# Performance work log

Hardware: AMD Instinct MI355X
Metric: run time of the kernel (lower is better)

## Reference

```python
import jax, jax.numpy as jnp
import numpy as np

EPS = 1e-5


def setup_inputs() -> dict:
    key = jax.random.key(0)
    ks = jax.random.split(key, 6)
    B, IN, OUT = 32768, 128, 2048
    return {
        "x": jax.random.normal(ks[0], (B, IN), dtype=jnp.float32),
        "y": jax.random.normal(ks[1], (B, OUT), dtype=jnp.float32),
        "linear_w": jax.random.normal(ks[2], (OUT, IN), dtype=jnp.float32) * (1.0 / np.sqrt(IN)),
        "linear_b": jax.random.normal(ks[3], (OUT,), dtype=jnp.float32) * 0.02,
        "norm_w": jax.random.uniform(ks[4], (OUT,), dtype=jnp.float32),
        "norm_b": jax.random.normal(ks[5], (OUT,), dtype=jnp.float32) * 0.02,
    }


def reference(x, y, linear_w, linear_b, norm_w, norm_b):
    # Linear: [B, IN] @ [IN, OUT] + b -> [B, OUT]
    h = jnp.einsum("bi,oi->bo", x, linear_w) + linear_b
    # Instance norm per row over the feature dim (biased variance, matching kernel)
    mean = jnp.mean(h, axis=-1, keepdims=True)
    var = jnp.mean(h * h, axis=-1, keepdims=True) - mean * mean
    inv_std = jax.lax.rsqrt(var + EPS)
    normed = (h - mean) * inv_std * norm_w + norm_b
    # Fused add then mul with second tensor
    return (normed + y) * y
```

## Files before the change

### kernel.cpp

```cpp
#include <hip/hip_runtime.h>
#include <hip/hip_bf16.h>
#include <cstdint>
#include <cstddef>


#define IN_DIM  128
#define OUT_DIM 2048
#define ROWS    16
#define EPS     1e-5f

typedef short  short8  __attribute__((ext_vector_type(8)));
typedef float  floatx4 __attribute__((ext_vector_type(4)));

__device__ __forceinline__ unsigned short f2bf(float f) {
    union { float f; unsigned int u; } v; v.f = f;
    unsigned int u = v.u;
    u += 0x7fffu + ((u >> 16) & 1u);
    return (unsigned short)(u >> 16);
}

__global__ void convert_w_kernel(const float* __restrict__ w,
                                 unsigned short* __restrict__ wbf, int n) {
    int i = (blockIdx.x * blockDim.x + threadIdx.x) * 4;
    if (i < n) {
        float4 v = *(const float4*)(w + i);
        ushort4 o;
        o.x = f2bf(v.x); o.y = f2bf(v.y); o.z = f2bf(v.z); o.w = f2bf(v.w);
        *(ushort4*)(wbf + i) = o;
    }
}

__global__ __launch_bounds__(512)
void fused_linear_norm_kernel(const float* __restrict__ x,
                              const float* __restrict__ y,
                              const unsigned short* __restrict__ wbf,
                              const float* __restrict__ lb,
                              const float* __restrict__ nw,
                              const float* __restrict__ nb,
                              float* __restrict__ out) {
    const int tid  = threadIdx.x;
    const int wave = tid >> 6;
    const int lane = tid & 63;
    const int l15  = lane & 15;
    const int quad = lane >> 4;
    const int row0 = blockIdx.x * ROWS;

    short8 afrag[4];
    {
        const float* xr = x + (size_t)(row0 + l15) * IN_DIM + quad * 8;
        #pragma unroll
        for (int s = 0; s < 4; ++s) {
            float4 p0 = *(const float4*)(xr + s * 32);
            float4 p1 = *(const float4*)(xr + s * 32 + 4);
            short8 a;
            a[0] = (short)f2bf(p0.x); a[1] = (short)f2bf(p0.y);
            a[2] = (short)f2bf(p0.z); a[3] = (short)f2bf(p0.w);
            a[4] = (short)f2bf(p1.x); a[5] = (short)f2bf(p1.y);
            a[6] = (short)f2bf(p1.z); a[7] = (short)f2bf(p1.w);
            afrag[s] = a;
        }
    }

    floatx4 acc[16];
    const int c0 = wave * 256;
    #pragma unroll
    for (int t = 0; t < 16; ++t) {
        acc[t] = (floatx4){0.f, 0.f, 0.f, 0.f};
        const unsigned short* wp = wbf + (size_t)(c0 + t * 16 + l15) * IN_DIM + quad * 8;
        #pragma unroll
        for (int s = 0; s < 4; ++s) {
            short8 b = *(const short8*)(wp + s * 32);
            acc[t] = __builtin_amdgcn_mfma_f32_16x16x32_bf16(afrag[s], b, acc[t], 0, 0, 0);
        }
    }

    float s1[4] = {0.f, 0.f, 0.f, 0.f};
    float s2[4] = {0.f, 0.f, 0.f, 0.f};
    #pragma unroll
    for (int t = 0; t < 16; ++t) {
        int col = c0 + t * 16 + l15;
        float bv = lb[col];
        #pragma unroll
        for (int r = 0; r < 4; ++r) {
            float h = acc[t][r] + bv;
            acc[t][r] = h;
            s1[r] += h;
            s2[r] += h * h;
        }
    }

    #pragma unroll
    for (int off = 1; off < 16; off <<= 1) {
        #pragma unroll
        for (int r = 0; r < 4; ++r) {
            s1[r] += __shfl_xor(s1[r], off);
            s2[r] += __shfl_xor(s2[r], off);
        }
    }

    __shared__ float red1[8][ROWS];
    __shared__ float red2[8][ROWS];
    __shared__ float smean[ROWS], sinv[ROWS];
    if (l15 == 0) {
        #pragma unroll
        for (int r = 0; r < 4; ++r) {
            red1[wave][quad * 4 + r] = s1[r];
            red2[wave][quad * 4 + r] = s2[r];
        }
    }
    __syncthreads();
    if (tid < ROWS) {
        float t1 = 0.f, t2 = 0.f;
        #pragma unroll
        for (int w = 0; w < 8; ++w) { t1 += red1[w][tid]; t2 += red2[w][tid]; }
        float mean = t1 * (1.0f / OUT_DIM);
        float var  = t2 * (1.0f / OUT_DIM) - mean * mean;
        smean[tid] = mean;
        sinv[tid]  = rsqrtf(var + EPS);
    }
    __syncthreads();

    float mean[4], inv[4];
    #pragma unroll
    for (int r = 0; r < 4; ++r) {
        mean[r] = smean[quad * 4 + r];
        inv[r]  = sinv[quad * 4 + r];
    }

    __shared__ float stage[8][ROWS][68];
    #pragma unroll
    for (int c = 0; c < 4; ++c) {
        #pragma unroll
        for (int tl = 0; tl < 4; ++tl) {
            const int t   = c * 4 + tl;
            const int col = c0 + t * 16 + l15;
            const float gw = nw[col];
            const float gb = nb[col];
            #pragma unroll
            for (int r = 0; r < 4; ++r) {
                const float normed = (acc[t][r] - mean[r]) * inv[r] * gw + gb;
                stage[wave][quad * 4 + r][tl * 16 + l15] = normed;
            }
        }
        __asm__ volatile("s_waitcnt lgkmcnt(0)" ::: "memory");
        #pragma unroll
        for (int i = 0; i < 4; ++i) {
            const int rl = i * 4 + quad;
            const float4 v = *(const float4*)&stage[wave][rl][l15 * 4];
            const size_t idx = (size_t)(row0 + rl) * OUT_DIM + (c0 + c * 64 + l15 * 4);
            const float4 yv = *(const float4*)(y + idx);
            float4 o;
            o.x = (v.x + yv.x) * yv.x;
            o.y = (v.y + yv.y) * yv.y;
            o.z = (v.z + yv.z) * yv.z;
            o.w = (v.w + yv.w) * yv.w;
            *(float4*)(out + idx) = o;
        }
    }
}

extern "C" void kernel_launch(void* const* d_in, const int* in_sizes, int n_in,
                              void* d_out, int out_size, void* d_ws, size_t ws_size,
                              hipStream_t stream) {
    const float* x  = (const float*)d_in[0];
    const float* y  = (const float*)d_in[1];
    const float* lw = (const float*)d_in[2];
    const float* lb = (const float*)d_in[3];
    const float* nw = (const float*)d_in[4];
    const float* nb = (const float*)d_in[5];
    float* out = (float*)d_out;
    unsigned short* wbf = (unsigned short*)d_ws;

    const int wn = OUT_DIM * IN_DIM;
    convert_w_kernel<<<wn / 4 / 256, 256, 0, stream>>>(lw, wbf, wn);

    const int nblocks = 32768 / ROWS;
    fused_linear_norm_kernel<<<nblocks, 512, 0, stream>>>(x, y, wbf, lb, nw, nb, out);
}
```

Before: 544.7 us.

## Prefetch y into LDS via async global_load_lds overlapping the MFMA loop

Issues asynchronous global-to-LDS loads of the block's y tile, interleaved with the GEMM MFMA loop, so the y fetch overlaps compute. The epilogue then reads y from LDS and writes the output directly as scalar stores, dropping the float4 LDS staging. The large y buffer in LDS (~131KB) limits the CU to one block, and the scalar stores are less coalesced than the old float4 writes.

```diff
diff --git a/kernel.cpp b/kernel.cpp
--- a/kernel.cpp
+++ b/kernel.cpp
@@ -1,5 +1,4 @@
 #include <hip/hip_runtime.h>
-#include <hip/hip_bf16.h>
 #include <cstdint>
 #include <cstddef>
 
@@ -7,6 +6,7 @@
 #define IN_DIM  128
 #define OUT_DIM 2048
 #define ROWS    16
+#define YPITCH  2052
 #define EPS     1e-5f
 
 typedef short  short8  __attribute__((ext_vector_type(8)));
@@ -45,6 +45,11 @@
     const int quad = lane >> 4;
     const int row0 = blockIdx.x * ROWS;
 
+    __shared__ float ylds[ROWS * YPITCH];
+    __shared__ float red1[8][ROWS];
+    __shared__ float red2[8][ROWS];
+    __shared__ float smean[ROWS], sinv[ROWS];
+
     short8 afrag[4];
     {
         const float* xr = x + (size_t)(row0 + l15) * IN_DIM + quad * 8;
@@ -63,6 +68,7 @@
 
     floatx4 acc[16];
     const int c0 = wave * 256;
+    const float* ybase = y + (size_t)row0 * OUT_DIM;
     #pragma unroll
     for (int t = 0; t < 16; ++t) {
         acc[t] = (floatx4){0.f, 0.f, 0.f, 0.f};
@@ -71,6 +77,15 @@
         for (int s = 0; s < 4; ++s) {
             short8 b = *(const short8*)(wp + s * 32);
             acc[t] = __builtin_amdgcn_mfma_f32_16x16x32_bf16(afrag[s], b, acc[t], 0, 0, 0);
+        }
+        {
+            const int r   = 2 * wave + (t >> 3);
+            const int seg = t & 7;
+            const float* gp = ybase + (size_t)r * OUT_DIM + seg * 256 + lane * 4;
+            float* lp = &ylds[r * YPITCH + seg * 256];
+            __builtin_amdgcn_global_load_lds(
+                (const __attribute__((address_space(1))) void*)gp,
+                (__attribute__((address_space(3))) void*)lp, 16, 0, 0);
         }
     }
 
@@ -98,9 +113,6 @@
         }
     }
 
-    __shared__ float red1[8][ROWS];
-    __shared__ float red2[8][ROWS];
-    __shared__ float smean[ROWS], sinv[ROWS];
     if (l15 == 0) {
         #pragma unroll
         for (int r = 0; r < 4; ++r) {
@@ -118,6 +130,7 @@
         smean[tid] = mean;
         sinv[tid]  = rsqrtf(var + EPS);
     }
+    __asm__ volatile("s_waitcnt vmcnt(0)" ::: "memory");
     __syncthreads();
 
     float mean[4], inv[4];
@@ -127,34 +140,18 @@
         inv[r]  = sinv[quad * 4 + r];
     }
 
-    __shared__ float stage[8][ROWS][68];
     #pragma unroll
-    for (int c = 0; c < 4; ++c) {
+    for (int t = 0; t < 16; ++t) {
+        const int col = c0 + t * 16 + l15;
+        const float gw = nw[col];
+        const float gb = nb[col];
         #pragma unroll
-        for (int tl = 0; tl < 4; ++tl) {
-            const int t   = c * 4 + tl;
-            const int col = c0 + t * 16 + l15;
-            const float gw = nw[col];
-            const float gb = nb[col];
-            #pragma unroll
-            for (int r = 0; r < 4; ++r) {
-                const float normed = (acc[t][r] - mean[r]) * inv[r] * gw + gb;
-                stage[wave][quad * 4 + r][tl * 16 + l15] = normed;
-            }
-        }
-        __asm__ volatile("s_waitcnt lgkmcnt(0)" ::: "memory");
-        #pragma unroll
-        for (int i = 0; i < 4; ++i) {
-            const int rl = i * 4 + quad;
-            const float4 v = *(const float4*)&stage[wave][rl][l15 * 4];
-            const size_t idx = (size_t)(row0 + rl) * OUT_DIM + (c0 + c * 64 + l15 * 4);
-            const float4 yv = *(const float4*)(y + idx);
-            float4 o;
-            o.x = (v.x + yv.x) * yv.x;
-            o.y = (v.y + yv.y) * yv.y;
-            o.z = (v.z + yv.z) * yv.z;
-            o.w = (v.w + yv.w) * yv.w;
-            *(float4*)(out + idx) = o;
+        for (int r = 0; r < 4; ++r) {
+            const int rl = quad * 4 + r;
+            const float normed = (acc[t][r] - mean[r]) * inv[r] * gw + gb;
+            const float yv = ylds[rl * YPITCH + col];
+            const float o  = (normed + yv) * yv;
+            out[(size_t)(row0 + rl) * OUT_DIM + col] = o;
         }
     }
 }
```

After: 545.3 us. No clear change (+0.1%).
